# Kernel tuning notes

Measured on AMD Instinct MI355X. Metric: run time of the kernel, lower is better.

Reference implementation:

```python
import jax, jax.numpy as jnp
import numpy as np

N = 8192
RANK_RATIO = 1.0


def setup_inputs() -> dict:
    key = jax.random.key(0)
    k1, k2, k3 = jax.random.split(key, 3)
    logit = jax.random.normal(k1, (N, 1), dtype=jnp.float32)
    status = jax.random.randint(k2, (N,), 0, 2).astype(jnp.float32)  # event indicator in {0,1}
    time = jax.random.uniform(k3, (N,), dtype=jnp.float32) * 10.0    # survival times
    status_time = jnp.stack([status, time], axis=1)  # [N, 2]
    return {"logit": logit, "status_time": status_time}


def reference(logit, status_time):
    status = status_time[:, 0]
    time = status_time[:, 1]
    lg = -logit.squeeze()  # [N]

    # Comparable pair (i, j): time[i] < time[j] and status[i] == 1.
    # i is the 'low' index (shorter, uncensored time), j is the 'high' index.
    mask = (time[:, None] < time[None, :]) & (status[:, None] == 1.0)  # [N, N]
    # rank term: relu(1 - lg[high] + lg[low])^2 over comparable pairs
    hinge = jnp.maximum(1.0 - lg[None, :] + lg[:, None], 0.0)
    sq = hinge * hinge
    n_pairs = jnp.maximum(jnp.sum(mask), 1)  # mean over selected pairs
    rank_loss = jnp.sum(jnp.where(mask, sq, 0.0)) / n_pairs.astype(sq.dtype)

    uncensor_part = time - lg
    censor_part = jnp.maximum(uncensor_part, 0.0)
    reg_term = (1.0 - status) * censor_part + status * uncensor_part
    reg_loss = jnp.mean(reg_term * reg_term)

    return RANK_RATIO * rank_loss + (1.0 - RANK_RATIO) * reg_loss
```

## Files before the change

### kernel.cpp

```cpp
#include <hip/hip_runtime.h>


constexpr int N_      = 8192;
constexpr int BLK     = 256;
constexpr int JCHUNK  = 512;
constexpr int NBI     = N_ / BLK;
constexpr int NJC     = N_ / JCHUNK;
constexpr int GRID    = NBI * NJC;

__global__ __launch_bounds__(BLK) void svm_partial(
        const float* __restrict__ logit,
        const float* __restrict__ st,
        float* __restrict__ psum,
        int* __restrict__ pcnt) {
    __shared__ float lg_s[JCHUNK];
    __shared__ float tm_s[JCHUNK];

    const int bi = blockIdx.x % NBI;
    const int bj = blockIdx.x / NBI;
    const int j0 = bj * JCHUNK;

    for (int t = threadIdx.x; t < JCHUNK; t += BLK) {
        lg_s[t] = -logit[j0 + t];
        tm_s[t] = st[2 * (j0 + t) + 1];
    }
    __syncthreads();

    const int   i   = bi * BLK + (int)threadIdx.x;
    const float lgi = -logit[i];
    const float sti = st[2 * i];
    const float tmi = st[2 * i + 1];

    float sum = 0.0f;
    int   cnt = 0;
    if (sti == 1.0f) {
        const float base = 1.0f + lgi;
        #pragma unroll 8
        for (int j = 0; j < JCHUNK; ++j) {
            float h  = fmaxf(base - lg_s[j], 0.0f);
            bool  m  = tmi < tm_s[j];
            float hm = m ? h : 0.0f;
            sum = fmaf(hm, hm, sum);
            cnt += (int)m;
        }
    }

    for (int off = 32; off > 0; off >>= 1) {
        sum += __shfl_down(sum, off, 64);
        cnt += __shfl_down(cnt, off, 64);
    }
    __shared__ float wsum[BLK / 64];
    __shared__ int   wcnt[BLK / 64];
    const int lane = threadIdx.x & 63;
    const int wid  = threadIdx.x >> 6;
    if (lane == 0) { wsum[wid] = sum; wcnt[wid] = cnt; }
    __syncthreads();
    if (threadIdx.x == 0) {
        float s = 0.0f; int c = 0;
        for (int w = 0; w < BLK / 64; ++w) { s += wsum[w]; c += wcnt[w]; }
        psum[blockIdx.x] = s;
        pcnt[blockIdx.x] = c;
    }
}

__global__ __launch_bounds__(GRID) void svm_final(
        const float* __restrict__ psum,
        const int* __restrict__ pcnt,
        float* __restrict__ out) {
    float s = psum[threadIdx.x];
    int   c = pcnt[threadIdx.x];
    for (int off = 32; off > 0; off >>= 1) {
        s += __shfl_down(s, off, 64);
        c += __shfl_down(c, off, 64);
    }
    __shared__ float wsum[GRID / 64];
    __shared__ int   wcnt[GRID / 64];
    const int lane = threadIdx.x & 63;
    const int wid  = threadIdx.x >> 6;
    if (lane == 0) { wsum[wid] = s; wcnt[wid] = c; }
    __syncthreads();
    if (threadIdx.x == 0) {
        float S = 0.0f; int C = 0;
        for (int w = 0; w < GRID / 64; ++w) { S += wsum[w]; C += wcnt[w]; }
        out[0] = S / (float)max(C, 1);
    }
}

extern "C" void kernel_launch(void* const* d_in, const int* in_sizes, int n_in,
                              void* d_out, int out_size, void* d_ws, size_t ws_size,
                              hipStream_t stream) {
    const float* logit = (const float*)d_in[0];
    const float* st    = (const float*)d_in[1];
    float* psum = (float*)d_ws;
    int*   pcnt = (int*)((float*)d_ws + GRID);

    svm_partial<<<GRID, BLK, 0, stream>>>(logit, st, psum, pcnt);
    svm_final<<<1, GRID, 0, stream>>>(psum, pcnt, (float*)d_out);
}
```

Baseline: 20.12 us.

## Loop over i uniformly per wave and fuse final reduction via atomic counter

```diff
diff --git a/kernel.cpp b/kernel.cpp
--- a/kernel.cpp
+++ b/kernel.cpp
@@ -1,88 +1,88 @@
 #include <hip/hip_runtime.h>
 
 
-constexpr int N_      = 8192;
-constexpr int BLK     = 256;
-constexpr int JCHUNK  = 512;
-constexpr int NBI     = N_ / BLK;
-constexpr int NJC     = N_ / JCHUNK;
-constexpr int GRID    = NBI * NJC;
+constexpr int N_   = 8192;
+constexpr int BLK  = 256;
+constexpr int NJB  = N_ / BLK;
+constexpr int NIC  = 32;
+constexpr int ICH  = N_ / NIC;
+constexpr int GRID = NJB * NIC;
 
-__global__ __launch_bounds__(BLK) void svm_partial(
+__global__ __launch_bounds__(BLK) void svm_fused(
         const float* __restrict__ logit,
         const float* __restrict__ st,
         float* __restrict__ psum,
-        int* __restrict__ pcnt) {
-    __shared__ float lg_s[JCHUNK];
-    __shared__ float tm_s[JCHUNK];
+        int*   __restrict__ pcnt,
+        unsigned int* __restrict__ counter,
+        float* __restrict__ out) {
+    const int jb = blockIdx.x & (NJB - 1);
+    const int ic = blockIdx.x / NJB;
+    const int j  = jb * BLK + (int)threadIdx.x;
 
-    const int bi = blockIdx.x % NBI;
-    const int bj = blockIdx.x / NBI;
-    const int j0 = bj * JCHUNK;
+    const float lj  = logit[j];
+    const float tmj = st[2 * j + 1];
 
-    for (int t = threadIdx.x; t < JCHUNK; t += BLK) {
-        lg_s[t] = -logit[j0 + t];
-        tm_s[t] = st[2 * (j0 + t) + 1];
-    }
-    __syncthreads();
-
-    const int   i   = bi * BLK + (int)threadIdx.x;
-    const float lgi = -logit[i];
-    const float sti = st[2 * i];
-    const float tmi = st[2 * i + 1];
+    const uint2* __restrict__ stu = (const uint2*)st;
 
     float sum = 0.0f;
     int   cnt = 0;
-    if (sti == 1.0f) {
-        const float base = 1.0f + lgi;
-        #pragma unroll 8
-        for (int j = 0; j < JCHUNK; ++j) {
-            float h  = fmaxf(base - lg_s[j], 0.0f);
-            bool  m  = tmi < tm_s[j];
-            float hm = m ? h : 0.0f;
+
+    const int i0 = ic * ICH;
+    #pragma unroll 4
+    for (int k = 0; k < ICH; ++k) {
+        const int   i  = i0 + k;
+        const uint2 sv = stu[i];
+        const float li = logit[i];
+        if (sv.x == 0x3f800000u) {
+            const float tmi = __uint_as_float(sv.y);
+            const float t   = (1.0f - li) + lj;
+            const bool  m   = tmi < tmj;
+            const bool  ok  = m && (t > 0.0f);
+            const float hm  = ok ? t : 0.0f;
             sum = fmaf(hm, hm, sum);
-            cnt += (int)m;
+            cnt += (int)__popcll(__ballot(m));
         }
     }
 
-    for (int off = 32; off > 0; off >>= 1) {
+    for (int off = 32; off > 0; off >>= 1)
         sum += __shfl_down(sum, off, 64);
-        cnt += __shfl_down(cnt, off, 64);
-    }
+
     __shared__ float wsum[BLK / 64];
     __shared__ int   wcnt[BLK / 64];
+    __shared__ bool  last;
     const int lane = threadIdx.x & 63;
     const int wid  = threadIdx.x >> 6;
     if (lane == 0) { wsum[wid] = sum; wcnt[wid] = cnt; }
     __syncthreads();
     if (threadIdx.x == 0) {
-        float s = 0.0f; int c = 0;
-        for (int w = 0; w < BLK / 64; ++w) { s += wsum[w]; c += wcnt[w]; }
+        float s = wsum[0] + wsum[1] + wsum[2] + wsum[3];
+        int   c = wcnt[0] + wcnt[1] + wcnt[2] + wcnt[3];
         psum[blockIdx.x] = s;
         pcnt[blockIdx.x] = c;
+        __threadfence();
+        unsigned int old = atomicAdd(counter, 1u);
+        last = (old == GRID - 1);
     }
-}
+    __syncthreads();
 
-__global__ __launch_bounds__(GRID) void svm_final(
-        const float* __restrict__ psum,
-        const int* __restrict__ pcnt,
-        float* __restrict__ out) {
-    float s = psum[threadIdx.x];
-    int   c = pcnt[threadIdx.x];
-    for (int off = 32; off > 0; off >>= 1) {
-        s += __shfl_down(s, off, 64);
-        c += __shfl_down(c, off, 64);
-    }
-    __shared__ float wsum[GRID / 64];
-    __shared__ int   wcnt[GRID / 64];
-    const int lane = threadIdx.x & 63;
-    const int wid  = threadIdx.x >> 6;
-    if (lane == 0) { wsum[wid] = s; wcnt[wid] = c; }
-    __syncthreads();
-    if (threadIdx.x == 0) {
-        float S = 0.0f; int C = 0;
-        for (int w = 0; w < GRID / 64; ++w) { S += wsum[w]; C += wcnt[w]; }
-        out[0] = S / (float)max(C, 1);
+    if (last) {
+        __threadfence();
+        float s = 0.0f; int c = 0;
+        for (int t = (int)threadIdx.x; t < GRID; t += BLK) {
+            s += psum[t];
+            c += pcnt[t];
+        }
+        for (int off = 32; off > 0; off >>= 1) {
+            s += __shfl_down(s, off, 64);
+            c += __shfl_down(c, off, 64);
+        }
+        if (lane == 0) { wsum[wid] = s; wcnt[wid] = c; }
+        __syncthreads();
+        if (threadIdx.x == 0) {
+            float S = wsum[0] + wsum[1] + wsum[2] + wsum[3];
+            int   C = wcnt[0] + wcnt[1] + wcnt[2] + wcnt[3];
+            out[0] = S / (float)(C > 0 ? C : 1);
+        }
     }
 }
 
@@ -91,9 +91,12 @@
                               hipStream_t stream) {
     const float* logit = (const float*)d_in[0];
     const float* st    = (const float*)d_in[1];
-    float* psum = (float*)d_ws;
-    int*   pcnt = (int*)((float*)d_ws + GRID);
 
-    svm_partial<<<GRID, BLK, 0, stream>>>(logit, st, psum, pcnt);
-    svm_final<<<1, GRID, 0, stream>>>(psum, pcnt, (float*)d_out);
+    float*        psum    = (float*)d_ws;
+    int*          pcnt    = (int*)((char*)d_ws + GRID * 4);
+    unsigned int* counter = (unsigned int*)((char*)d_ws + GRID * 8);
+
+    hipMemsetAsync(counter, 0, sizeof(unsigned int), stream);
+    svm_fused<<<GRID, BLK, 0, stream>>>(logit, st, psum, pcnt, counter,
+                                        (float*)d_out);
 }
```

After: 49.74 us. 2.47x slower.
